# Performance work log

Hardware: AMD Instinct MI355X
Metric: run time of the kernel (lower is better)

Reference implementation:

```python
import jax, jax.numpy as jnp
import numpy as np

EPS1 = 1e-8
EPS2 = 1e-5
H_BW = 1.0  # bandwidth h
MSE_W = 1.0
CTX_W = 1.0
PERC_W = 0.02


def _contextual_similarity(out_feat, tgt_feat):
    """Batched contextual similarity (Mechrez et al. 2018).

    out_feat, tgt_feat: [B, C, Hf, Wf]. Returns scalar (mean over batch).
    Matches the torch loop-over-samples / loop-over-target-vectors math,
    fully vectorized as one batched pairwise-cosine + softmax + max.
    """
    B, C = out_feat.shape[0], out_feat.shape[1]
    # X, Y: [B, N, C] with N = Hf*Wf spatial positions
    X = out_feat.reshape(B, C, -1).transpose(0, 2, 1)
    Y = tgt_feat.reshape(B, C, -1).transpose(0, 2, 1)
    X = X - X.mean(axis=1, keepdims=True)  # center per channel over positions
    Y = Y - Y.mean(axis=1, keepdims=True)
    xn = jnp.linalg.norm(X, axis=2)  # [B, N]
    yn = jnp.linalg.norm(Y, axis=2)  # [B, N]
    # cosine distance d[b, x, y] = 1 - <X_x, Y_y> / (|X_x||Y_y| + eps1)
    S = jnp.einsum('bxc,byc->bxy', X, Y)
    d = 1.0 - S / (xn[:, :, None] * yn[:, None, :] + EPS1)
    # normalize by min over target vectors y (torch: dxy.min(dim=0) with dxy [Ny, Nx])
    d_ = d / (d.min(axis=2, keepdims=True) + EPS2)
    w = jnp.exp((1.0 - d_) / H_BW)
    c = w / w.sum(axis=2, keepdims=True)  # softmax over y per x
    # torch: cxy.max(dim=1)[0].mean() -> max over x for each y, mean over y
    CS = c.max(axis=1).mean(axis=1)  # [B]
    return CS.mean()


def _mse(a, b):
    return jnp.mean((a - b) ** 2)


def setup_inputs() -> dict:
    key = jax.random.key(0)
    k1, k2, k3, k4 = jax.random.split(key, 4)
    outputs = jax.random.normal(k1, (4, 3, 256, 256), dtype=jnp.float32)
    targets = jax.random.normal(k2, (4, 3, 256, 256), dtype=jnp.float32)
    output_features = jax.random.normal(k3, (4, 256, 64, 64), dtype=jnp.float32)
    target_features = jax.random.normal(k4, (4, 256, 64, 64), dtype=jnp.float32)
    return {"outputs": outputs, "targets": targets,
            "output_features": output_features, "target_features": target_features}


def reference(outputs, targets, output_features, target_features):
    loss = MSE_W * _mse(outputs, targets)
    loss = loss - CTX_W * jnp.log(_contextual_similarity(output_features, target_features))
    loss = loss + PERC_W * _mse(output_features, target_features)
    return loss
```

## Files before the change

kernel.cpp:

```cpp
#include <hip/hip_runtime.h>
#include <hip/hip_bf16.h>
#include <cstdint>

#define EPS2f 1e-5f

typedef __bf16 bf16x8 __attribute__((ext_vector_type(8)));
typedef float floatx4 __attribute__((ext_vector_type(4)));
typedef _Float16 half8 __attribute__((ext_vector_type(8)));
typedef __fp16 fp16x2 __attribute__((ext_vector_type(2)));

static constexpr int Bn = 4, Cn = 256, Nn = 4096;

static constexpr size_t MSE1P = 0;
static constexpr size_t MSE2P = 256;
static constexpr size_t CSP   = 1536;
static constexpr size_t MEANX = 2560;
static constexpr size_t MEANY = 3584;
static constexpr size_t IXN   = 4608;
static constexpr size_t IYN   = 20992;
static constexpr size_t DMIN  = 37376;
static constexpr size_t RSUM  = 53760;
static constexpr size_t XCO   = 70144;
static constexpr size_t YCO   = 70144 + 2097152;
static constexpr size_t SOFF  = 70144 + 2 * 2097152;

__device__ __forceinline__ unsigned short f2bf(float f) {
    unsigned u = __float_as_uint(f);
    u += 0x7fffu + ((u >> 16) & 1u);
    return (unsigned short)(u >> 16);
}

__global__ __launch_bounds__(256) void prep1(const float4* __restrict__ outs,
                                             const float4* __restrict__ tgts,
                                             const float4* __restrict__ of4,
                                             const float4* __restrict__ tf4,
                                             float* __restrict__ ws) {
    const int bid = blockIdx.x, t = threadIdx.x;
    __shared__ float red[12];
    if (bid < 1024) {
        const int c = bid & 255, b = bid >> 8;
        const float4* po = of4 + ((size_t)b * Cn + c) * (Nn / 4);
        const float4* pt = tf4 + ((size_t)b * Cn + c) * (Nn / 4);
        float so = 0.f, st = 0.f, sq = 0.f;
        for (int i = t; i < 1024; i += 256) {
            float4 o = po[i], q = pt[i];
            so += o.x + o.y + o.z + o.w;
            st += q.x + q.y + q.z + q.w;
            float dx = o.x - q.x, dy = o.y - q.y, dz = o.z - q.z, dw = o.w - q.w;
            sq += dx * dx + dy * dy + dz * dz + dw * dw;
        }
        for (int m = 1; m < 64; m <<= 1) {
            so += __shfl_xor(so, m); st += __shfl_xor(st, m); sq += __shfl_xor(sq, m);
        }
        if ((t & 63) == 0) { int w = t >> 6; red[w * 3] = so; red[w * 3 + 1] = st; red[w * 3 + 2] = sq; }
        __syncthreads();
        if (t == 0) {
            so = red[0] + red[3] + red[6] + red[9];
            st = red[1] + red[4] + red[7] + red[10];
            sq = red[2] + red[5] + red[8] + red[11];
            ws[MEANX + b * Cn + c] = so * (1.f / 4096.f);
            ws[MEANY + b * Cn + c] = st * (1.f / 4096.f);
            ws[MSE2P + bid] = sq;
        }
    } else if (bid < 1216) {
        const int base = bid - 1024;
        float sq = 0.f;
        for (int i = base * 256 + t; i < 196608; i += 192 * 256) {
            float4 a = outs[i], b4 = tgts[i];
            float dx = a.x - b4.x, dy = a.y - b4.y, dz = a.z - b4.z, dw = a.w - b4.w;
            sq += dx * dx + dy * dy + dz * dz + dw * dw;
        }
        for (int m = 1; m < 64; m <<= 1) sq += __shfl_xor(sq, m);
        if ((t & 63) == 0) red[t >> 6] = sq;
        __syncthreads();
        if (t == 0) ws[MSE1P + base] = red[0] + red[1] + red[2] + red[3];
    } else {
        const int i = (bid - 1216) * 256 + t;
        ws[DMIN + i] = (i < 16384) ? __builtin_inff() : 0.f;
    }
}

__global__ __launch_bounds__(256) void center_fused(const float* __restrict__ ofeat,
                                                    const float* __restrict__ tfeat,
                                                    float* __restrict__ ws) {
    const int b = blockIdx.y, nb = blockIdx.x, z = blockIdx.z;
    const float* feat = z ? tfeat : ofeat;
    const float* mean = ws + (z ? MEANY : MEANX);
    unsigned short* outb = (unsigned short*)(ws + (z ? YCO : XCO));
    float* inv = ws + (z ? IYN : IXN);
    __shared__ float mean_s[256];
    __shared__ float sq_s[256];
    const int t = threadIdx.x;
    mean_s[t] = mean[b * Cn + t];
    __syncthreads();
    const int pos = t & 63, cg = t >> 6;
    const int n = nb * 64 + pos;
    const float* fb = feat + (size_t)b * Cn * Nn;
    unsigned short* ob = outb + ((size_t)b * Nn + n) * Cn;
    float ss = 0.f;
    for (int c0 = cg * 64; c0 < cg * 64 + 64; c0 += 8) {
        unsigned short tmp[8];
        #pragma unroll
        for (int u = 0; u < 8; ++u) {
            float v = fb[(size_t)(c0 + u) * Nn + n] - mean_s[c0 + u];
            ss += v * v;
            tmp[u] = f2bf(v);
        }
        uint4 pk;
        pk.x = (unsigned)tmp[0] | ((unsigned)tmp[1] << 16);
        pk.y = (unsigned)tmp[2] | ((unsigned)tmp[3] << 16);
        pk.z = (unsigned)tmp[4] | ((unsigned)tmp[5] << 16);
        pk.w = (unsigned)tmp[6] | ((unsigned)tmp[7] << 16);
        *(uint4*)(ob + c0) = pk;
    }
    sq_s[t] = ss;
    __syncthreads();
    if (t < 64) {
        float s = sq_s[t] + sq_s[t + 64] + sq_s[t + 128] + sq_s[t + 192];
        inv[(size_t)b * Nn + nb * 64 + t] = 1.f / sqrtf(s);
    }
}

__global__ __launch_bounds__(256) void gemm_store(const unsigned short* __restrict__ Xc,
                                                  const unsigned short* __restrict__ Yc,
                                                  const float* __restrict__ ixn,
                                                  const float* __restrict__ iyn,
                                                  float* __restrict__ dmin,
                                                  _Float16* __restrict__ S) {
    __shared__ __align__(16) unsigned short T[128 * 128];
    __shared__ float ixn_s[128], iyn_s[128];

    const int t = threadIdx.x;
    const int bx = blockIdx.x, by = blockIdx.y, b = blockIdx.z;
    const size_t nb = (size_t)b * Nn;

    if (t < 128) ixn_s[t] = ixn[nb + bx * 128 + t];
    else iyn_s[t - 128] = iyn[nb + by * 128 + (t - 128)];
    __syncthreads();

    const int wid = t >> 6, lane = t & 63;
    const int wm = wid >> 1, wn = wid & 1;
    const int lr = lane & 15, lq = lane >> 4;

    const unsigned short* Abase = Xc + (nb + bx * 128 + wm * 64 + lr) * Cn + lq * 8;
    const unsigned short* Bbase = Yc + (nb + by * 128 + wn * 64 + lr) * Cn + lq * 8;

    floatx4 acc[4][4];
    #pragma unroll
    for (int i = 0; i < 4; i++)
        #pragma unroll
        for (int j = 0; j < 4; j++) acc[i][j] = (floatx4){0.f, 0.f, 0.f, 0.f};

    bf16x8 af[2][4], bv[2][4];
    #pragma unroll
    for (int i = 0; i < 4; i++) {
        af[0][i] = *(const bf16x8*)(Abase + i * 16 * Cn);
        bv[0][i] = *(const bf16x8*)(Bbase + i * 16 * Cn);
    }
    #pragma unroll
    for (int ks = 0; ks < 8; ks++) {
        const int cur = ks & 1, nxt = cur ^ 1;
        if (ks < 7) {
            #pragma unroll
            for (int i = 0; i < 4; i++) {
                af[nxt][i] = *(const bf16x8*)(Abase + i * 16 * Cn + (ks + 1) * 32);
                bv[nxt][i] = *(const bf16x8*)(Bbase + i * 16 * Cn + (ks + 1) * 32);
            }
        }
        #pragma unroll
        for (int i = 0; i < 4; i++)
            #pragma unroll
            for (int j = 0; j < 4; j++)
                acc[i][j] = __builtin_amdgcn_mfma_f32_16x16x32_bf16(af[cur][i], bv[cur][j], acc[i][j], 0, 0, 0);
    }

    float rmin[16];
    #pragma unroll
    for (int k = 0; k < 16; k++) rmin[k] = __builtin_inff();
    float ix[16];
    #pragma unroll
    for (int i = 0; i < 4; i++)
        #pragma unroll
        for (int r = 0; r < 4; r++) ix[i * 4 + r] = ixn_s[wm * 64 + i * 16 + lq * 4 + r];

    #pragma unroll
    for (int i = 0; i < 4; i++) {
        const int xlocal = wm * 64 + i * 16 + lq * 4;
        #pragma unroll
        for (int j = 0; j < 4; j++) {
            const int ylocal = wn * 64 + j * 16 + lr;
            const float iy = iyn_s[ylocal];
            float c0 = acc[i][j][0] * ix[i * 4 + 0] * iy;
            float c1 = acc[i][j][1] * ix[i * 4 + 1] * iy;
            float c2 = acc[i][j][2] * ix[i * 4 + 2] * iy;
            float c3 = acc[i][j][3] * ix[i * 4 + 3] * iy;
            rmin[i * 4 + 0] = fminf(rmin[i * 4 + 0], 1.f - c0);
            rmin[i * 4 + 1] = fminf(rmin[i * 4 + 1], 1.f - c1);
            rmin[i * 4 + 2] = fminf(rmin[i * 4 + 2], 1.f - c2);
            rmin[i * 4 + 3] = fminf(rmin[i * 4 + 3], 1.f - c3);
            fp16x2 p0 = __builtin_amdgcn_cvt_pkrtz(c0, c1);
            fp16x2 p1 = __builtin_amdgcn_cvt_pkrtz(c2, c3);
            *(float2*)(T + ylocal * 128 + xlocal) =
                make_float2(__builtin_bit_cast(float, p0), __builtin_bit_cast(float, p1));
        }
    }
    #pragma unroll
    for (int m = 1; m < 16; m <<= 1)
        #pragma unroll
        for (int k = 0; k < 16; k++) rmin[k] = fminf(rmin[k], __shfl_xor(rmin[k], m));
    if (lr == 0) {
        #pragma unroll
        for (int i = 0; i < 4; i++)
            #pragma unroll
            for (int r = 0; r < 4; r++)
                atomicMin((int*)&dmin[nb + bx * 128 + wm * 64 + i * 16 + lq * 4 + r],
                          __float_as_int(rmin[i * 4 + r]));
    }
    __syncthreads();

    #pragma unroll
    for (int p = 0; p < 8; p++) {
        const int yl = wid * 32 + p * 4 + (lane >> 4);
        const int ch = lane & 15;
        uint4 v = *(const uint4*)(T + yl * 128 + ch * 8);
        *(uint4*)(S + (nb + by * 128 + yl) * (size_t)Nn + bx * 128 + ch * 8) = v;
    }
}

__global__ __launch_bounds__(256) void b1_rsum(const _Float16* __restrict__ S,
                                               const float* __restrict__ dmin,
                                               float* __restrict__ rsum) {
    __shared__ float red[32 * 65];
    const int t = threadIdx.x;
    const int x0 = blockIdx.x * 64, ys = blockIdx.y, b = blockIdx.z;
    const int chunk = t & 7, yg = t >> 3;
    const int xbase = x0 + chunk * 8;
    const size_t gb = (size_t)b * Nn;

    float invd[8], av[8];
    #pragma unroll
    for (int u = 0; u < 8; u++) {
        float dm = dmin[gb + xbase + u];
        invd[u] = 1.f / (dm + EPS2f);
        av[u] = 1.f - invd[u];
    }
    float s[8];
    #pragma unroll
    for (int u = 0; u < 8; u++) s[u] = 0.f;

    for (int k = 0; k < 16; k++) {
        const int y = ys * 512 + yg + 32 * k;
        half8 hv = *(const half8*)(S + (gb + y) * Nn + xbase);
        #pragma unroll
        for (int u = 0; u < 8; u++)
            s[u] += __expf(fmaf((float)hv[u], invd[u], av[u]));
    }
    #pragma unroll
    for (int u = 0; u < 8; u++) red[yg * 65 + chunk * 8 + u] = s[u];
    __syncthreads();
    if (t < 64) {
        float rs = 0.f;
        #pragma unroll 8
        for (int g = 0; g < 32; g++) rs += red[g * 65 + t];
        atomicAdd(&rsum[gb + x0 + t], rs);
    }
}

__global__ __launch_bounds__(256) void b2_cmax(const _Float16* __restrict__ S,
                                               const float* __restrict__ dmin,
                                               const float* __restrict__ rsum,
                                               float* __restrict__ csp) {
    __shared__ float ps[512 * 20];
    __shared__ float red2[16];
    const int t = threadIdx.x, b = blockIdx.y;
    const size_t gb = (size_t)b * Nn;
    for (int i = t; i < Nn; i += 256) {
        float iv = 1.f / (dmin[gb + i] + EPS2f);
        float gg = 1.f - iv - __logf(rsum[gb + i]);
        int c = i >> 3, e = i & 7;
        ps[c * 20 + e * 2] = iv;
        ps[c * 20 + e * 2 + 1] = gg;
    }
    __syncthreads();

    const int lanegrp = t & 15, yloc = t >> 4;
    const int y = blockIdx.x * 16 + yloc;
    const _Float16* Sy = S + (gb + y) * Nn;

    float cm = 0.f;
    for (int k = 0; k < 32; k++) {
        const int chunk = lanegrp + 16 * k;
        half8 hv = *(const half8*)(Sy + chunk * 8);
        const float* pp = &ps[chunk * 20];
        float4 p01 = *(const float4*)(pp);
        float4 p23 = *(const float4*)(pp + 4);
        float4 p45 = *(const float4*)(pp + 8);
        float4 p67 = *(const float4*)(pp + 12);
        float iv[8] = {p01.x, p01.z, p23.x, p23.z, p45.x, p45.z, p67.x, p67.z};
        float gg[8] = {p01.y, p01.w, p23.y, p23.w, p45.y, p45.w, p67.y, p67.w};
        #pragma unroll
        for (int u = 0; u < 8; u++)
            cm = fmaxf(cm, __expf(fmaf((float)hv[u], iv[u], gg[u])));
    }
    #pragma unroll
    for (int m = 1; m < 16; m <<= 1) cm = fmaxf(cm, __shfl_xor(cm, m));
    if (lanegrp == 0) red2[yloc] = cm;
    __syncthreads();
    if (t == 0) {
        float s2 = 0.f;
        #pragma unroll
        for (int i = 0; i < 16; i++) s2 += red2[i];
        csp[b * 256 + blockIdx.x] = s2;
    }
}

__global__ __launch_bounds__(256) void finalize_kernel(const float* __restrict__ ws,
                                                       float* __restrict__ out) {
    const int t = threadIdx.x;
    float s1 = 0.f, s2 = 0.f, s3 = 0.f;
    if (t < 192) s1 = ws[MSE1P + t];
    for (int i = t; i < 1024; i += 256) { s2 += ws[MSE2P + i]; s3 += ws[CSP + i]; }
    for (int m = 1; m < 64; m <<= 1) {
        s1 += __shfl_xor(s1, m); s2 += __shfl_xor(s2, m); s3 += __shfl_xor(s3, m);
    }
    __shared__ float red[12];
    if ((t & 63) == 0) { int w = t >> 6; red[w * 3] = s1; red[w * 3 + 1] = s2; red[w * 3 + 2] = s3; }
    __syncthreads();
    if (t == 0) {
        s1 = red[0] + red[3] + red[6] + red[9];
        s2 = red[1] + red[4] + red[7] + red[10];
        s3 = red[2] + red[5] + red[8] + red[11];
        float cs = s3 * (1.f / 16384.f);
        out[0] = s1 * (1.f / 786432.f) - logf(cs) + 0.02f * s2 * (1.f / 4194304.f);
    }
}

extern "C" void kernel_launch(void* const* d_in, const int* in_sizes, int n_in,
                              void* d_out, int out_size, void* d_ws, size_t ws_size,
                              hipStream_t stream) {
    const float* outputs = (const float*)d_in[0];
    const float* targets = (const float*)d_in[1];
    const float* ofeat   = (const float*)d_in[2];
    const float* tfeat   = (const float*)d_in[3];
    float* ws  = (float*)d_ws;
    float* out = (float*)d_out;

    unsigned short* Xc = (unsigned short*)(ws + XCO);
    unsigned short* Yc = (unsigned short*)(ws + YCO);
    _Float16* S = (_Float16*)(ws + SOFF);

    prep1<<<1344, 256, 0, stream>>>((const float4*)outputs, (const float4*)targets,
                                    (const float4*)ofeat, (const float4*)tfeat, ws);
    center_fused<<<dim3(Nn / 64, Bn, 2), 256, 0, stream>>>(ofeat, tfeat, ws);
    gemm_store<<<dim3(Nn / 128, Nn / 128, Bn), 256, 0, stream>>>(Xc, Yc, ws + IXN, ws + IYN,
                                                                 ws + DMIN, S);
    b1_rsum<<<dim3(64, 8, Bn), 256, 0, stream>>>(S, ws + DMIN, ws + RSUM);
    b2_cmax<<<dim3(Nn / 16, Bn), 256, 0, stream>>>(S, ws + DMIN, ws + RSUM, ws + CSP);
    finalize_kernel<<<1, 256, 0, stream>>>(ws, out);
}
```

Baseline: 285.7 us.

## Stage GEMM operand tiles through double-buffered LDS and swizzle transpose buffer

The GEMM kernel now loads each A/B k-slice cooperatively into double-buffered shared memory instead of having every wave fetch its fragments straight from global memory. This removes duplicate global loads across waves that share rows. The row-min reduction is moved before the transposed fp16 store, and the transpose buffer uses an XOR swizzle to cut LDS bank conflicts. The cost is extra LDS traffic and a barrier on every k-step.

```diff
diff --git a/kernel.cpp b/kernel.cpp
--- a/kernel.cpp
+++ b/kernel.cpp
@@ -127,7 +127,7 @@
                                                   const float* __restrict__ iyn,
                                                   float* __restrict__ dmin,
                                                   _Float16* __restrict__ S) {
-    __shared__ __align__(16) unsigned short T[128 * 128];
+    __shared__ __align__(16) unsigned short smem[16384];
     __shared__ float ixn_s[128], iyn_s[128];
 
     const int t = threadIdx.x;
@@ -136,14 +136,20 @@
 
     if (t < 128) ixn_s[t] = ixn[nb + bx * 128 + t];
     else iyn_s[t - 128] = iyn[nb + by * 128 + (t - 128)];
-    __syncthreads();
 
     const int wid = t >> 6, lane = t & 63;
     const int wm = wid >> 1, wn = wid & 1;
     const int lr = lane & 15, lq = lane >> 4;
-
-    const unsigned short* Abase = Xc + (nb + bx * 128 + wm * 64 + lr) * Cn + lq * 8;
-    const unsigned short* Bbase = Yc + (nb + by * 128 + wn * 64 + lr) * Cn + lq * 8;
+    const int srow = t >> 2, sq = t & 3;
+
+    const unsigned short* Ag = Xc + (nb + bx * 128) * Cn;
+    const unsigned short* Bg = Yc + (nb + by * 128) * Cn;
+    const unsigned short* Ga0 = Ag + (size_t)srow * Cn + sq * 8;
+    const unsigned short* Ga1 = Ag + (size_t)(srow + 64) * Cn + sq * 8;
+    const unsigned short* Gb0 = Bg + (size_t)srow * Cn + sq * 8;
+    const unsigned short* Gb1 = Bg + (size_t)(srow + 64) * Cn + sq * 8;
+    const int wA0 = (sq * 128 + srow) * 8;
+    const int wA1 = (sq * 128 + srow + 64) * 8;
 
     floatx4 acc[4][4];
     #pragma unroll
@@ -151,37 +157,77 @@
         #pragma unroll
         for (int j = 0; j < 4; j++) acc[i][j] = (floatx4){0.f, 0.f, 0.f, 0.f};
 
-    bf16x8 af[2][4], bv[2][4];
-    #pragma unroll
-    for (int i = 0; i < 4; i++) {
-        af[0][i] = *(const bf16x8*)(Abase + i * 16 * Cn);
-        bv[0][i] = *(const bf16x8*)(Bbase + i * 16 * Cn);
-    }
+    {
+        uint4 a0 = *(const uint4*)Ga0, a1 = *(const uint4*)Ga1;
+        uint4 b0 = *(const uint4*)Gb0, b1 = *(const uint4*)Gb1;
+        *(uint4*)(smem + wA0) = a0;
+        *(uint4*)(smem + wA1) = a1;
+        *(uint4*)(smem + 4096 + wA0) = b0;
+        *(uint4*)(smem + 4096 + wA1) = b1;
+    }
+    __syncthreads();
+
     #pragma unroll
     for (int ks = 0; ks < 8; ks++) {
-        const int cur = ks & 1, nxt = cur ^ 1;
+        const int cur = (ks & 1) * 8192, nxt = 8192 - cur;
+        uint4 a0, a1, b0, b1;
         if (ks < 7) {
-            #pragma unroll
-            for (int i = 0; i < 4; i++) {
-                af[nxt][i] = *(const bf16x8*)(Abase + i * 16 * Cn + (ks + 1) * 32);
-                bv[nxt][i] = *(const bf16x8*)(Bbase + i * 16 * Cn + (ks + 1) * 32);
-            }
-        }
+            a0 = *(const uint4*)(Ga0 + (ks + 1) * 32);
+            a1 = *(const uint4*)(Ga1 + (ks + 1) * 32);
+            b0 = *(const uint4*)(Gb0 + (ks + 1) * 32);
+            b1 = *(const uint4*)(Gb1 + (ks + 1) * 32);
+        }
+        bf16x8 af[4], bv[4];
+        #pragma unroll
+        for (int i = 0; i < 4; i++)
+            af[i] = *(const bf16x8*)(smem + cur + (lq * 128 + wm * 64 + i * 16 + lr) * 8);
+        #pragma unroll
+        for (int j = 0; j < 4; j++)
+            bv[j] = *(const bf16x8*)(smem + cur + 4096 + (lq * 128 + wn * 64 + j * 16 + lr) * 8);
         #pragma unroll
         for (int i = 0; i < 4; i++)
             #pragma unroll
             for (int j = 0; j < 4; j++)
-                acc[i][j] = __builtin_amdgcn_mfma_f32_16x16x32_bf16(af[cur][i], bv[cur][j], acc[i][j], 0, 0, 0);
-    }
-
+                acc[i][j] = __builtin_amdgcn_mfma_f32_16x16x32_bf16(af[i], bv[j], acc[i][j], 0, 0, 0);
+        if (ks < 7) {
+            *(uint4*)(smem + nxt + wA0) = a0;
+            *(uint4*)(smem + nxt + wA1) = a1;
+            *(uint4*)(smem + nxt + 4096 + wA0) = b0;
+            *(uint4*)(smem + nxt + 4096 + wA1) = b1;
+            __syncthreads();
+        }
+    }
+
+    float ix[16];
+    #pragma unroll
+    for (int i = 0; i < 4; i++)
+        #pragma unroll
+        for (int r = 0; r < 4; r++) ix[i * 4 + r] = ixn_s[wm * 64 + i * 16 + lq * 4 + r];
     float rmin[16];
     #pragma unroll
     for (int k = 0; k < 16; k++) rmin[k] = __builtin_inff();
-    float ix[16];
     #pragma unroll
     for (int i = 0; i < 4; i++)
         #pragma unroll
-        for (int r = 0; r < 4; r++) ix[i * 4 + r] = ixn_s[wm * 64 + i * 16 + lq * 4 + r];
+        for (int j = 0; j < 4; j++) {
+            const float iy = iyn_s[wn * 64 + j * 16 + lr];
+            #pragma unroll
+            for (int r = 0; r < 4; r++)
+                rmin[i * 4 + r] = fminf(rmin[i * 4 + r], 1.f - acc[i][j][r] * ix[i * 4 + r] * iy);
+        }
+    #pragma unroll
+    for (int m = 1; m < 16; m <<= 1)
+        #pragma unroll
+        for (int k = 0; k < 16; k++) rmin[k] = fminf(rmin[k], __shfl_xor(rmin[k], m));
+    if (lr == 0) {
+        #pragma unroll
+        for (int i = 0; i < 4; i++)
+            #pragma unroll
+            for (int r = 0; r < 4; r++)
+                atomicMin((int*)&dmin[nb + bx * 128 + wm * 64 + i * 16 + lq * 4 + r],
+                          __float_as_int(rmin[i * 4 + r]));
+    }
+    __syncthreads();
 
     #pragma unroll
     for (int i = 0; i < 4; i++) {
@@ -194,27 +240,11 @@
             float c1 = acc[i][j][1] * ix[i * 4 + 1] * iy;
             float c2 = acc[i][j][2] * ix[i * 4 + 2] * iy;
             float c3 = acc[i][j][3] * ix[i * 4 + 3] * iy;
-            rmin[i * 4 + 0] = fminf(rmin[i * 4 + 0], 1.f - c0);
-            rmin[i * 4 + 1] = fminf(rmin[i * 4 + 1], 1.f - c1);
-            rmin[i * 4 + 2] = fminf(rmin[i * 4 + 2], 1.f - c2);
-            rmin[i * 4 + 3] = fminf(rmin[i * 4 + 3], 1.f - c3);
             fp16x2 p0 = __builtin_amdgcn_cvt_pkrtz(c0, c1);
             fp16x2 p1 = __builtin_amdgcn_cvt_pkrtz(c2, c3);
-            *(float2*)(T + ylocal * 128 + xlocal) =
+            *(float2*)(smem + ylocal * 128 + (xlocal ^ ((ylocal & 15) * 8))) =
                 make_float2(__builtin_bit_cast(float, p0), __builtin_bit_cast(float, p1));
         }
-    }
-    #pragma unroll
-    for (int m = 1; m < 16; m <<= 1)
-        #pragma unroll
-        for (int k = 0; k < 16; k++) rmin[k] = fminf(rmin[k], __shfl_xor(rmin[k], m));
-    if (lr == 0) {
-        #pragma unroll
-        for (int i = 0; i < 4; i++)
-            #pragma unroll
-            for (int r = 0; r < 4; r++)
-                atomicMin((int*)&dmin[nb + bx * 128 + wm * 64 + i * 16 + lq * 4 + r],
-                          __float_as_int(rmin[i * 4 + r]));
     }
     __syncthreads();
 
@@ -222,7 +252,7 @@
     for (int p = 0; p < 8; p++) {
         const int yl = wid * 32 + p * 4 + (lane >> 4);
         const int ch = lane & 15;
-        uint4 v = *(const uint4*)(T + yl * 128 + ch * 8);
+        uint4 v = *(const uint4*)(smem + yl * 128 + ((ch * 8) ^ ((yl & 15) * 8)));
         *(uint4*)(S + (nb + by * 128 + yl) * (size_t)Nn + bx * 128 + ch * 8) = v;
     }
 }
```

Result: faster. 237.9 us (-16.7%).
